# Kernel tuning notes

Hardware: AMD Instinct MI355X
Metric: run time of the kernel (lower is better)

Reference implementation:

```python
import jax, jax.numpy as jnp
import numpy as np
import math

Q_DIM = 1024
K_DIM = 1024
ATT_DIM = 1024
POS_DIM = 64
B, NQ, NK = 4, 2048, 2048
EPS = 1e-5


def _ln(x, g, b):
    m = jnp.mean(x, axis=-1, keepdims=True)
    v = jnp.var(x, axis=-1, keepdims=True)
    return (x - m) * jax.lax.rsqrt(v + EPS) * g + b


def _sinpos(n, dim):
    # SinPos: exp = 2*arange(dim//2)/dim; pos = p * 10000**-exp; cat(pos, pos+pi/2); sin
    e = 2.0 * jnp.arange(dim // 2, dtype=jnp.float32) / dim      # [dim/2]
    p = jnp.arange(n, dtype=jnp.float32)[:, None]                # [n,1]
    ph = p * jnp.power(10000.0, -e)[None, :]                     # [n,dim/2]
    return jnp.sin(jnp.concatenate([ph, ph + math.pi / 2], axis=1))  # [n,dim]


def setup_inputs() -> dict:
    key = jax.random.key(0)
    ks = jax.random.split(key, 8)
    s = 0.02
    return {
        "q": jax.random.normal(ks[0], (B, NQ, Q_DIM), jnp.float32),
        "k": jax.random.normal(ks[1], (B, NK, K_DIM), jnp.float32),
        "Wq": jax.random.normal(ks[2], (Q_DIM, ATT_DIM), jnp.float32) * s,
        "bq": jnp.zeros((ATT_DIM,), jnp.float32),
        "Wk": jax.random.normal(ks[3], (K_DIM, ATT_DIM), jnp.float32) * s,
        "bk": jnp.zeros((ATT_DIM,), jnp.float32),
        "Wv": jax.random.normal(ks[4], (K_DIM, ATT_DIM), jnp.float32) * s,
        "bv": jnp.zeros((ATT_DIM,), jnp.float32),
        "gq": jnp.ones((ATT_DIM,), jnp.float32), "betaq": jnp.zeros((ATT_DIM,), jnp.float32),
        "gk": jnp.ones((ATT_DIM,), jnp.float32), "betak": jnp.zeros((ATT_DIM,), jnp.float32),
        "gv": jnp.ones((ATT_DIM,), jnp.float32), "betav": jnp.zeros((ATT_DIM,), jnp.float32),
        "Wp": jax.random.normal(ks[5], (POS_DIM, POS_DIM), jnp.float32) * s,
        "bp": jnp.zeros((POS_DIM,), jnp.float32),
    }


def reference(q, k, Wq, bq, Wk, bk, Wv, bv, gq, betaq, gk, betak, gv, betav, Wp, bp):
    qn = _ln(q @ Wq + bq, gq, betaq)          # [B,NQ,D]
    vn = _ln(k @ Wv + bv, gv, betav)          # [B,NK,D]
    kn = _ln(k @ Wk + bk, gk, betak)          # [B,NK,D]
    pos = _sinpos(NK, POS_DIM)                # [NK,P]

    # attention 1: Q=qn, K=kn, V=pos
    s1 = jnp.einsum('bnd,bjd->bnj', qn, kn) * (1.0 / math.sqrt(ATT_DIM))
    a1 = jax.nn.softmax(s1, axis=-1)          # [B,NQ,NK]
    x = jnp.einsum('bnj,jp->bnp', a1, pos)    # [B,NQ,P]

    # pos_net (Linear)
    x = x @ Wp + bp                           # [B,NQ,P]

    # attention 2: Q=x, K=pos, V=vn
    s2 = jnp.einsum('bnp,jp->bnj', x, pos) * (1.0 / math.sqrt(POS_DIM))
    a2 = jax.nn.softmax(s2, axis=-1)          # [B,NQ,NK]
    out = jnp.einsum('bnj,bjd->bnd', a2, vn)  # [B,NQ,D]

    att = jnp.stack([a1, a2], axis=1)         # [B,2,NQ,NK] == torch.cat over head dim
    return out, att
```

## Files before the change

### kernel.cpp

```cpp
#include <hip/hip_runtime.h>
#include <math.h>
#include <stdint.h>


typedef _Float16 f16;
typedef _Float16 f16x4 __attribute__((ext_vector_type(4)));
typedef _Float16 f16x8 __attribute__((ext_vector_type(8)));
typedef float f32x4 __attribute__((ext_vector_type(4)));

static constexpr int CB  = 4;
static constexpr int CNQ = 2048;
static constexpr int CNK = 2048;
static constexpr int CD  = 1024;
static constexpr int CP  = 64;

static __device__ __forceinline__ void async16(const f16* gp, f16* lp) {
  __builtin_amdgcn_global_load_lds(
      (const __attribute__((address_space(1))) void*)(uintptr_t)gp,
      (__attribute__((address_space(3))) void*)(uint32_t)(uintptr_t)lp,
      16, 0, 0);
}

__global__ __launch_bounds__(256) void prep_kernel(
    const float* __restrict__ q, const float* __restrict__ k,
    const float* __restrict__ Wq, const float* __restrict__ Wk,
    const float* __restrict__ Wv,
    f16* __restrict__ q16, f16* __restrict__ k16,
    f16* __restrict__ WqT, f16* __restrict__ WkvT,
    f16* __restrict__ posb, f16* __restrict__ posTb) {
  const int b = blockIdx.x;
  if (b < 512) {
    int tid = b * 256 + threadIdx.x;
    int p = tid >> 11;
    int j = tid & (CNK - 1);
    int i = p & 31;
    float ph = (float)j * powf(10000.0f, -(float)i * (1.0f / 32.0f));
    float v = (p < 32) ? sinf(ph) : cosf(ph);
    posb[j * CP + p]   = (f16)v;
    posTb[p * CNK + j] = (f16)v;
  } else if (b < 512 + 16384) {
    const int NF4 = CB * CNQ * CD / 4;
    int tid = (b - 512) * 256 + threadIdx.x;
    const float* src = (tid < NF4) ? q : k;
    f16* dst = (tid < NF4) ? q16 : k16;
    int i = (tid < NF4) ? tid : tid - NF4;
    float4 v = reinterpret_cast<const float4*>(src)[i];
    f16x4 o = {(f16)v.x, (f16)v.y, (f16)v.z, (f16)v.w};
    reinterpret_cast<f16x4*>(dst)[i] = o;
  } else {
    __shared__ float t[64][65];
    const int idx = b - 16896;
    const int z = idx >> 8;
    const int rem = idx & 255;
    const float* W = (z == 0) ? Wq : (z == 1) ? Wk : Wv;
    f16* WT = (z == 0) ? WqT : (z == 1) ? WkvT : WkvT + 1024 * 1024;
    int k0 = (rem & 15) * 64, n0 = (rem >> 4) * 64;
    int tx = threadIdx.x & 63, ty = threadIdx.x >> 6;
#pragma unroll
    for (int i = 0; i < 16; i++)
      t[ty + 4 * i][tx] = W[(size_t)(k0 + ty + 4 * i) * CD + n0 + tx];
    __syncthreads();
#pragma unroll
    for (int i = 0; i < 16; i++)
      WT[(size_t)(n0 + 4 * i + ty) * CD + k0 + tx] = (f16)t[tx][ty + 4 * i];
  }
}

template <int BM, int BN>
__device__ __forceinline__ void gemm_core2(
    const f16* __restrict__ Ab, const f16* __restrict__ Bb,
    int lda, int ldb, int K, int m0, int n0, f16* sm,
    f32x4 (&acc)[BM / 32][4]) {
  constexpr int FM = BM / 32;
  constexpr int TI = (BM + BN) / 64;
  constexpr int bufsz = (BM + BN) * 64;
  const int tid = threadIdx.x;
  const int lane = tid & 63, wid = tid >> 6;
  const int wr = wid >> 2, wc = wid & 3;
  const int lrow = lane & 15, kg = lane >> 4;

  auto stage = [&](int i, int kt, int buf) {
    const int s = i * 512 + tid;
    const int row = s >> 3;
    const int cb = (s & 7) << 4;
    const int scb = cb ^ ((row & 7) << 4);
    const f16* src = (i < BM / 64)
        ? Ab + (size_t)(m0 + row) * lda + kt * 64 + (scb >> 1)
        : Bb + (size_t)(n0 + row - BM) * ldb + kt * 64 + (scb >> 1);
    async16(src, &sm[buf * bufsz + s * 8]);
  };

  const int NTk = K >> 6;
#pragma unroll
  for (int i = 0; i < TI; i++) stage(i, 0, 0);

  for (int t = 0; t < NTk; ++t) {
    const int cur = t & 1;
    if (t + 1 < NTk) {
#pragma unroll
      for (int i = 0; i < TI; i++) stage(i, t + 1, cur ^ 1);
      if constexpr (TI == 8) asm volatile("s_waitcnt vmcnt(8)" ::: "memory");
      else                   asm volatile("s_waitcnt vmcnt(6)" ::: "memory");
    } else {
      asm volatile("s_waitcnt vmcnt(0)" ::: "memory");
    }
    __builtin_amdgcn_s_barrier();

    const f16* smA = sm + cur * bufsz;
    const f16* smB = smA + BM * 64;
#pragma unroll
    for (int kk = 0; kk < 2; ++kk) {
      const int Cb = kk * 64 + kg * 16;
      f16x8 af[FM], bf[4];
#pragma unroll
      for (int m = 0; m < FM; ++m) {
        const int ar = wr * (BM / 2) + m * 16 + lrow;
        af[m] = *reinterpret_cast<const f16x8*>(
            &smA[ar * 64 + ((Cb ^ ((ar & 7) << 4)) >> 1)]);
      }
#pragma unroll
      for (int n = 0; n < 4; ++n) {
        const int br = wc * 64 + n * 16 + lrow;
        bf[n] = *reinterpret_cast<const f16x8*>(
            &smB[br * 64 + ((Cb ^ ((br & 7) << 4)) >> 1)]);
      }
      __builtin_amdgcn_s_barrier();
      __builtin_amdgcn_s_setprio(1);
#pragma unroll
      for (int m = 0; m < FM; ++m)
#pragma unroll
        for (int n = 0; n < 4; ++n)
          acc[m][n] = __builtin_amdgcn_mfma_f32_16x16x32_f16(af[m], bf[n], acc[m][n], 0, 0, 0);
      __builtin_amdgcn_s_setprio(0);
      __builtin_amdgcn_s_barrier();
    }
  }
}

template <int BM, int BN>
__device__ __forceinline__ void epi_f16(
    f32x4 (&acc)[BM / 32][4], f16* sm, f16* Cp, int ldc, int m0, int n0) {
  const int tid = threadIdx.x, lane = tid & 63, wid = tid >> 6;
  const int wr = wid >> 2, wc = wid & 3;
  const int rbase = wr * (BM / 2) + (lane >> 4) * 4;
  const int cbase = wc * 64 + (lane & 15);
  __syncthreads();
#pragma unroll
  for (int mg = 0; mg < BM / 32; mg++)
#pragma unroll
    for (int n = 0; n < 4; n++)
#pragma unroll
      for (int r = 0; r < 4; r++)
        sm[(rbase + mg * 16 + r) * BN + cbase + n * 16] = (f16)acc[mg][n][r];
  __syncthreads();
  constexpr int CH = BM * BN / (512 * 8);
#pragma unroll
  for (int c = 0; c < CH; c++) {
    const int idx = c * 512 + tid;
    const int row = idx / (BN / 8);
    const int cole = (idx % (BN / 8)) * 8;
    f16x8 v = *reinterpret_cast<const f16x8*>(&sm[row * BN + cole]);
    *reinterpret_cast<f16x8*>(Cp + (size_t)(m0 + row) * ldc + n0 + cole) = v;
  }
}

template <int BM, int BN>
__device__ __forceinline__ void epi_exp(
    f32x4 (&acc)[BM / 32][4], f16* sm, float* psum, f16* Cp, int ldc,
    int m0, int n0, float scale, float* PSrow) {
  constexpr int SL = BN / 8;
  const int tid = threadIdx.x, lane = tid & 63, wid = tid >> 6;
  const int wr = wid >> 2, wc = wid & 3;
  const int rbase = wr * (BM / 2) + (lane >> 4) * 4;
  const int cbase = wc * 64 + (lane & 15);
  __syncthreads();
#pragma unroll
  for (int mg = 0; mg < BM / 32; mg++)
#pragma unroll
    for (int n = 0; n < 4; n++)
#pragma unroll
      for (int r = 0; r < 4; r++)
        sm[(rbase + mg * 16 + r) * BN + cbase + n * 16] =
            (f16)__expf(acc[mg][n][r] * scale);
  __syncthreads();
  constexpr int CH = BM * BN / (512 * 8);
#pragma unroll
  for (int c = 0; c < CH; c++) {
    const int idx = c * 512 + tid;
    const int row = idx / SL;
    const int cole = (idx % SL) * 8;
    f16x8 v = *reinterpret_cast<const f16x8*>(&sm[row * BN + cole]);
    *reinterpret_cast<f16x8*>(Cp + (size_t)(m0 + row) * ldc + n0 + cole) = v;
    float p = 0.f;
#pragma unroll
    for (int j = 0; j < 8; j++) p += (float)v[j];
#pragma unroll
    for (int o = 1; o < SL; o <<= 1) p += __shfl_xor(p, o);
    if ((lane & (SL - 1)) == 0) psum[row] = p;
  }
  __syncthreads();
  if (tid < BM) PSrow[tid] = psum[tid];
}

template <int BM, int BN>
__device__ __forceinline__ void epi_f32(
    f32x4 (&acc)[BM / 32][4], f16* smh, float* Cp, int ldc, int m0, int n0) {
  float* st = (float*)smh;
  const int tid = threadIdx.x, lane = tid & 63, wid = tid >> 6;
  const int wr = wid >> 2, wc = wid & 3;
  const int cbase = wc * 64 + (lane & 15);
#pragma unroll
  for (int half = 0; half < 2; half++) {
    __syncthreads();
    if (wr == half) {
#pragma unroll
      for (int mg = 0; mg < BM / 32; mg++)
#pragma unroll
        for (int r = 0; r < 4; r++) {
          const int rloc = (lane >> 4) * 4 + mg * 16 + r;
#pragma unroll
          for (int n = 0; n < 4; n++)
            st[rloc * BN + cbase + n * 16] = acc[mg][n][r];
        }
    }
    __syncthreads();
    constexpr int CH = (BM / 2) * BN / (512 * 4);
#pragma unroll
    for (int c = 0; c < CH; c++) {
      const int idx = c * 512 + tid;
      const int row = idx / (BN / 4);
      const int cole = (idx % (BN / 4)) * 4;
      float4 v = *reinterpret_cast<const float4*>(&st[row * BN + cole]);
      *reinterpret_cast<float4*>(
          Cp + (size_t)(m0 + half * (BM / 2) + row) * ldc + n0 + cole) = v;
    }
  }
}

__global__ __launch_bounds__(512) void gemmIn_kernel(
    const f16* __restrict__ q16, const f16* __restrict__ WqT, f16* __restrict__ tmpq,
    const f16* __restrict__ k16, const f16* __restrict__ WkvT, f16* __restrict__ tmp2) {
  __shared__ __attribute__((aligned(16))) f16 sm[2 * (128 + 256) * 64];
  const int b = blockIdx.x;
  const int swz = (b & 7) * 96 + (b >> 3);
  const f16 *A, *B;
  f16* C;
  int ldc, m0, n0;
  if (swz < 256) {
    const int bx = swz & 63, by = swz >> 6;
    A = q16; B = WqT; C = tmpq; ldc = 1024; m0 = bx * 128; n0 = by * 256;
  } else {
    const int idx = swz - 256;
    const int bx = idx & 63, by = idx >> 6;
    A = k16; B = WkvT; C = tmp2; ldc = 2048; m0 = bx * 128; n0 = by * 256;
  }
  f32x4 acc[4][4] = {};
  gemm_core2<128, 256>(A, B, 1024, 1024, 1024, m0, n0, sm, acc);
  epi_f16<128, 256>(acc, sm, C, ldc, m0, n0);
}

__global__ __launch_bounds__(512) void gemmS1_kernel(
    const f16* __restrict__ qn, const f16* __restrict__ kn,
    f16* __restrict__ e1, float* __restrict__ PS) {
  __shared__ __attribute__((aligned(16))) f16 sm[2 * (256 + 256) * 64];
  __shared__ float psum[256];
  const int b = blockIdx.x;
  const int swz = (b & 7) * 32 + (b >> 3);
  const int bz = swz >> 6;
  const int rem = swz & 63;
  const int bx = rem & 7, by = rem >> 3;
  const int m0 = bx * 256, n0 = by * 256;
  const f16* Ab = qn + (size_t)bz * 2048 * 1024;
  const f16* Bb = kn + (size_t)bz * 2048 * 2048;
  f16* Cp = e1 + (size_t)bz * 2048 * 2048;
  f32x4 acc[8][4] = {};
  gemm_core2<256, 256>(Ab, Bb, 1024, 2048, 1024, m0, n0, sm, acc);
  epi_exp<256, 256>(acc, sm, psum, Cp, 2048, m0, n0, 0.03125f,
                    PS + (size_t)by * (CB * CNQ) + bz * 2048 + m0);
}

__global__ __launch_bounds__(512) void gemmOut_kernel(
    const f16* __restrict__ e2, const f16* __restrict__ vnT, float* __restrict__ out) {
  __shared__ __attribute__((aligned(16))) f16 sm[2 * (128 + 256) * 64];
  const int b = blockIdx.x;
  const int swz = (b & 7) * 32 + (b >> 3);
  const int bz = swz >> 6;
  const int rem = swz & 63;
  const int bx = rem & 15, by = rem >> 4;
  const int m0 = bx * 128, n0 = by * 256;
  const f16* Ab = e2 + (size_t)bz * 2048 * 2048;
  const f16* Bb = vnT + (size_t)bz * 1024 * 2048;
  float* Cp = out + (size_t)bz * 2048 * 1024;
  f32x4 acc[4][4] = {};
  gemm_core2<128, 256>(Ab, Bb, 2048, 2048, 2048, m0, n0, sm, acc);
  epi_f32<128, 256>(acc, sm, Cp, 1024, m0, n0);
}

__global__ __launch_bounds__(256) void ln3_kernel(
    f16* __restrict__ tmpq, f16* __restrict__ tmp2, float* __restrict__ vstat,
    const float* __restrict__ bq, const float* __restrict__ gq, const float* __restrict__ beq,
    const float* __restrict__ bk, const float* __restrict__ gk, const float* __restrict__ bek,
    const float* __restrict__ bv) {
  __shared__ float rs_[4], rq_[4];
  const int z = blockIdx.y;
  f16* rp;
  const float *bias, *g, *beta;
  if (z == 0)      { rp = tmpq + (size_t)blockIdx.x * 1024;        bias = bq; g = gq; beta = beq; }
  else if (z == 1) { rp = tmp2 + (size_t)blockIdx.x * 2048;        bias = bk; g = gk; beta = bek; }
  else             { rp = tmp2 + (size_t)blockIdx.x * 2048 + 1024; bias = bv; g = nullptr; beta = nullptr; }
  const int t = threadIdx.x;
  f16x4 v = *reinterpret_cast<const f16x4*>(rp + t * 4);
  float y[4], s = 0.f, q = 0.f;
#pragma unroll
  for (int j = 0; j < 4; j++) {
    y[j] = (float)v[j] + bias[t * 4 + j];
    s += y[j]; q += y[j] * y[j];
  }
#pragma unroll
  for (int o = 32; o; o >>= 1) { s += __shfl_xor(s, o); q += __shfl_xor(q, o); }
  if ((t & 63) == 0) { rs_[t >> 6] = s; rq_[t >> 6] = q; }
  __syncthreads();
  s = rs_[0] + rs_[1] + rs_[2] + rs_[3];
  q = rq_[0] + rq_[1] + rq_[2] + rq_[3];
  const float mean = s * (1.0f / CD);
  const float rstd = rsqrtf(q * (1.0f / CD) - mean * mean + 1e-5f);
  if (z == 2) {
    if (t == 0) { vstat[blockIdx.x] = mean; vstat[CB * CNK + blockIdx.x] = rstd; }
    return;
  }
  f16x4 o;
#pragma unroll
  for (int j = 0; j < 4; j++) {
    int c = t * 4 + j;
    o[j] = (f16)((y[j] - mean) * rstd * g[c] + beta[c]);
  }
  *reinterpret_cast<f16x4*>(rp + t * 4) = o;
}

__global__ __launch_bounds__(256) void transposeLN_kernel(
    const f16* __restrict__ tmp2, f16* __restrict__ vnT,
    const float* __restrict__ vstat, const float* __restrict__ bv,
    const float* __restrict__ gv, const float* __restrict__ bev) {
  __shared__ f16 t[64][65];
  __shared__ float ms[64], rs[64];
  int n0 = blockIdx.x * 64, d0 = blockIdx.y * 64;
  size_t ibase = (size_t)blockIdx.z * CNK * 2048;
  size_t obase = (size_t)blockIdx.z * CNK * CD;
  int tx = threadIdx.x & 63, ty = threadIdx.x >> 6;
  const int tokbase = blockIdx.z * CNK + n0;
  if (threadIdx.x < 64) {
    ms[threadIdx.x] = vstat[tokbase + threadIdx.x];
    rs[threadIdx.x] = vstat[CB * CNK + tokbase + threadIdx.x];
  }
#pragma unroll
  for (int i = 0; i < 16; i++)
    t[ty + 4 * i][tx] = tmp2[ibase + (size_t)(n0 + ty + 4 * i) * 2048 + 1024 + d0 + tx];
  __syncthreads();
#pragma unroll
  for (int i = 0; i < 16; i++) {
    const int dim = d0 + 4 * i + ty;
    const float yv = (float)t[tx][ty + 4 * i] + bv[dim];
    vnT[obase + (size_t)dim * CNK + n0 + tx] =
        (f16)((yv - ms[tx]) * rs[tx] * gv[dim] + bev[dim]);
  }
}

__global__ __launch_bounds__(256) void xgemm_kernel(
    const f16* __restrict__ e1, const f16* __restrict__ posTb,
    const float* __restrict__ PS, float* __restrict__ xw, float* __restrict__ att) {
  constexpr int BM = 64, BN = 64;
  __shared__ __attribute__((aligned(16))) f16 As[BM * 32];
  __shared__ __attribute__((aligned(16))) f16 Bs[BN * 32];
  __shared__ float invs[BM];
  const int tid = threadIdx.x;
  const int lane = tid & 63;
  const int wave = tid >> 6;
  const int wr = wave >> 1, wc = wave & 1;
  const int m0 = blockIdx.x * BM;
  const int kbase = blockIdx.z * 1024;
  const int srow = lane >> 2;
  const int scol = (lane & 3) * 8;
  const int lrow = lane & 15;
  const int kg = lane >> 4;

  if (tid < BM) {
    float s = 0.f;
#pragma unroll
    for (int j = 0; j < 8; j++) s += PS[j * (CB * CNQ) + m0 + tid];
    invs[tid] = 1.0f / s;
  }

  const int bb = m0 >> 11, nloc = m0 & (CNQ - 1);
  float* attb = att + ((size_t)(bb << 1) * CNQ + nloc) * CNK + kbase;
  const int arow = tid >> 2, acol = (tid & 3) * 8;

  f32x4 acc[2][2] = {};
  for (int k0 = 0; k0 < 1024; k0 += 32) {
    __syncthreads();
#pragma unroll
    for (int i = wave; i < 8; i += 4) {
      if (i < 4)
        async16(e1 + (size_t)(m0 + i * 16 + srow) * CNK + kbase + k0 + scol, &As[i * 512]);
      else
        async16(posTb + (size_t)((i - 4) * 16 + srow) * CNK + kbase + k0 + scol,
                &Bs[(i - 4) * 512]);
    }
    __syncthreads();
    f16x8 af[2], bfr[2];
#pragma unroll
    for (int m = 0; m < 2; m++)
      af[m] = *reinterpret_cast<const f16x8*>(&As[(wr * 32 + m * 16 + lrow) * 32 + kg * 8]);
#pragma unroll
    for (int n = 0; n < 2; n++)
      bfr[n] = *reinterpret_cast<const f16x8*>(&Bs[(wc * 32 + n * 16 + lrow) * 32 + kg * 8]);
#pragma unroll
    for (int m = 0; m < 2; m++)
#pragma unroll
      for (int n = 0; n < 2; n++)
        acc[m][n] = __builtin_amdgcn_mfma_f32_16x16x32_f16(af[m], bfr[n], acc[m][n], 0, 0, 0);
    {
      const float iv = invs[arow];
      f16x8 v = *reinterpret_cast<const f16x8*>(&As[arow * 32 + acol]);
      float4 w0 = {(float)v[0] * iv, (float)v[1] * iv, (float)v[2] * iv, (float)v[3] * iv};
      float4 w1 = {(float)v[4] * iv, (float)v[5] * iv, (float)v[6] * iv, (float)v[7] * iv};
      float* ap = attb + (size_t)arow * CNK + k0 + acol;
      reinterpret_cast<float4*>(ap)[0] = w0;
      reinterpret_cast<float4*>(ap)[1] = w1;
    }
  }
  float* Cp = xw + (size_t)blockIdx.z * (CB * CNQ) * CP;
  const int crow = m0 + wr * 32 + (lane >> 4) * 4;
  const int ccol = wc * 32 + (lane & 15);
#pragma unroll
  for (int m = 0; m < 2; m++)
#pragma unroll
    for (int n = 0; n < 2; n++)
#pragma unroll
      for (int r = 0; r < 4; r++)
        Cp[(size_t)(crow + m * 16 + r) * CP + ccol + n * 16] = acc[m][n][r];
}

__global__ __launch_bounds__(512) void attn2_kernel(
    const float* __restrict__ xw, const float* __restrict__ Wp,
    const float* __restrict__ bp, const f16* __restrict__ posb,
    const float* __restrict__ PS, f16* __restrict__ e2,
    float* __restrict__ att) {
  __shared__ __attribute__((aligned(16))) f16 shm[32 * 2048 + 32 * 64];
  __shared__ float rsum4[4][32];
  __shared__ float invs[32];
  f16* e2lds = shm;
  f16* xpb = shm + 32 * 2048;
  float* xs = (float*)shm;
  float* Wps = (float*)shm + 32 * 64;
  const int tid = threadIdx.x, l = tid & 63, w = tid >> 6;
  const int r0 = blockIdx.x * 32;
  if (tid < 32) {
    float s = 0.f;
#pragma unroll
    for (int j = 0; j < 8; j++) s += PS[j * (CB * CNQ) + r0 + tid];
    invs[tid] = 1.0f / s;
  }
  __syncthreads();
  if (w < 2) {
#pragma unroll
    for (int i = 0; i < 16; i++) {
      const int row = w * 16 + i;
      const size_t gi = (size_t)(r0 + row) * CP + l;
      xs[row * 64 + l] = (xw[gi] + xw[(size_t)(CB * CNQ) * CP + gi]) * invs[row];
    }
#pragma unroll
    for (int i = w; i < 64; i += 2) Wps[i * 64 + l] = Wp[i * 64 + l];
  }
  const float bpl = bp[l];
  __syncthreads();
  if (w < 2) {
#pragma unroll 2
    for (int i = 0; i < 16; i++) {
      float a = bpl;
#pragma unroll 8
      for (int p = 0; p < 64; p++) a = fmaf(xs[(w * 16 + i) * 64 + p], Wps[p * 64 + l], a);
      xpb[(w * 16 + i) * 64 + l] = (f16)a;
    }
  }
  __syncthreads();
  const int rb = (w & 1) * 16, jh = w >> 1;
  const f16x8 af0 = *reinterpret_cast<const f16x8*>(&xpb[(rb + (l & 15)) * 64 + (l >> 4) * 8]);
  const f16x8 af1 = *reinterpret_cast<const f16x8*>(&xpb[(rb + (l & 15)) * 64 + 32 + (l >> 4) * 8]);
  float rs[4] = {0.f, 0.f, 0.f, 0.f};
  for (int jt = jh * 8; jt < jh * 8 + 8; jt++) {
#pragma unroll
    for (int q4 = 0; q4 < 4; q4++) {
      const int j = jt * 64 + q4 * 16 + (l & 15);
      const f16* pp = posb + (size_t)j * CP + (l >> 4) * 8;
      f16x8 b0 = *reinterpret_cast<const f16x8*>(pp);
      f16x8 b1 = *reinterpret_cast<const f16x8*>(pp + 32);
      f32x4 c = {};
      c = __builtin_amdgcn_mfma_f32_16x16x32_f16(af0, b0, c, 0, 0, 0);
      c = __builtin_amdgcn_mfma_f32_16x16x32_f16(af1, b1, c, 0, 0, 0);
#pragma unroll
      for (int r = 0; r < 4; r++) {
        float ev = __expf(c[r] * 0.125f);
        rs[r] += ev;
        e2lds[(rb + (l >> 4) * 4 + r) * 2048 + j] = (f16)ev;
      }
    }
  }
#pragma unroll
  for (int r = 0; r < 4; r++) {
#pragma unroll
    for (int o = 1; o < 16; o <<= 1) rs[r] += __shfl_xor(rs[r], o);
    if ((l & 15) == 0) rsum4[jh][rb + (l >> 4) * 4 + r] = rs[r];
  }
  __syncthreads();
  const int b = r0 >> 11, nloc = r0 & (CNQ - 1);
  float* attb = att + ((size_t)((b << 1) + 1) * CNQ + nloc) * CNK;
  f16* e2b = e2 + (size_t)r0 * CNK;
  for (int it = 0; it < 8; it++) {
    const int row = it * 4 + (tid >> 7);
    const int col = (tid & 127) * 16;
    const float iv = 1.0f / (rsum4[0][row] + rsum4[1][row] + rsum4[2][row] + rsum4[3][row]);
    const f16x8 a0 = *reinterpret_cast<const f16x8*>(&e2lds[row * 2048 + col]);
    const f16x8 a1 = *reinterpret_cast<const f16x8*>(&e2lds[row * 2048 + col + 8]);
    float4 w0 = {(float)a0[0] * iv, (float)a0[1] * iv, (float)a0[2] * iv, (float)a0[3] * iv};
    float4 w1 = {(float)a0[4] * iv, (float)a0[5] * iv, (float)a0[6] * iv, (float)a0[7] * iv};
    float4 w2 = {(float)a1[0] * iv, (float)a1[1] * iv, (float)a1[2] * iv, (float)a1[3] * iv};
    float4 w3 = {(float)a1[4] * iv, (float)a1[5] * iv, (float)a1[6] * iv, (float)a1[7] * iv};
    float* ap = attb + (size_t)row * CNK + col;
    reinterpret_cast<float4*>(ap)[0] = w0;
    reinterpret_cast<float4*>(ap)[1] = w1;
    reinterpret_cast<float4*>(ap)[2] = w2;
    reinterpret_cast<float4*>(ap)[3] = w3;
    f16x8 h0 = {(f16)w0.x, (f16)w0.y, (f16)w0.z, (f16)w0.w,
                (f16)w1.x, (f16)w1.y, (f16)w1.z, (f16)w1.w};
    f16x8 h1 = {(f16)w2.x, (f16)w2.y, (f16)w2.z, (f16)w2.w,
                (f16)w3.x, (f16)w3.y, (f16)w3.z, (f16)w3.w};
    f16* ep = e2b + (size_t)row * CNK + col;
    *reinterpret_cast<f16x8*>(ep)     = h0;
    *reinterpret_cast<f16x8*>(ep + 8) = h1;
  }
}

extern "C" void kernel_launch(void* const* d_in, const int* in_sizes, int n_in,
                              void* d_out, int out_size, void* d_ws, size_t ws_size,
                              hipStream_t stream) {
  (void)in_sizes; (void)n_in; (void)out_size; (void)ws_size;
  const float* q    = (const float*)d_in[0];
  const float* k    = (const float*)d_in[1];
  const float* Wq   = (const float*)d_in[2];
  const float* bq   = (const float*)d_in[3];
  const float* Wk   = (const float*)d_in[4];
  const float* bk   = (const float*)d_in[5];
  const float* Wv   = (const float*)d_in[6];
  const float* bv   = (const float*)d_in[7];
  const float* gq   = (const float*)d_in[8];
  const float* betaq= (const float*)d_in[9];
  const float* gk   = (const float*)d_in[10];
  const float* betak= (const float*)d_in[11];
  const float* gv   = (const float*)d_in[12];
  const float* betav= (const float*)d_in[13];
  const float* Wp   = (const float*)d_in[14];
  const float* bp   = (const float*)d_in[15];

  float* out = (float*)d_out;
  float* att = out + (size_t)CB * CNQ * CD;
  char* ws = (char*)d_ws;
  const size_t MB = 1ull << 20;

  f16* q16   = (f16*)(ws);
  f16* k16   = (f16*)(ws + 16 * MB);
  f16* e1    = (f16*)(ws);
  f16* e2    = (f16*)(ws);
  f16* WqT   = (f16*)(ws + 32 * MB);
  f16* WkvT  = (f16*)(ws + 34 * MB);
  f16* posb  = (f16*)(ws + 38 * MB);
  f16* posTb = (f16*)(ws + 38 * MB + 256 * 1024);
  float* xw  = (float*)(ws + 38 * MB + 512 * 1024);
  float* PS  = (float*)(ws + 42 * MB + 512 * 1024);
  float* vstat = (float*)(ws + 42 * MB + 768 * 1024);
  f16* tmpq  = (f16*)(ws + 43 * MB);
  f16* tmp2  = (f16*)(ws + 59 * MB);
  f16* vnT   = (f16*)(ws + 91 * MB);
  f16* qn = tmpq;
  f16* kn = tmp2;

  prep_kernel<<<512 + 16384 + 768, 256, 0, stream>>>(
      q, k, Wq, Wk, Wv, q16, k16, WqT, WkvT, posb, posTb);

  gemmIn_kernel<<<768, 512, 0, stream>>>(q16, WqT, tmpq, k16, WkvT, tmp2);
  ln3_kernel<<<dim3(CB * CNQ, 3), 256, 0, stream>>>(
      tmpq, tmp2, vstat, bq, gq, betaq, bk, gk, betak, bv);
  transposeLN_kernel<<<dim3(CNK / 64, CD / 64, CB), 256, 0, stream>>>(
      tmp2, vnT, vstat, bv, gv, betav);

  gemmS1_kernel<<<256, 512, 0, stream>>>(qn, kn, e1, PS);

  xgemm_kernel<<<dim3(CB * CNQ / 64, 1, 2), 256, 0, stream>>>(e1, posTb, PS, xw, att);
  attn2_kernel<<<CB * CNQ / 32, 512, 0, stream>>>(xw, Wp, bp, posb, PS, e2, att);

  gemmOut_kernel<<<256, 512, 0, stream>>>(e2, vnT, out);
}
```

Before: 292.5 us.

## Double-buffer xgemm, use nontemporal att stores, trim GEMM mainloop barriers

Rewrites xgemm to 512 threads with a swizzled, double-buffered async LDS pipeline over 64-wide K tiles. The normalized att1 write now happens after the GEMM and re-reads e1 from global memory instead of LDS. The shared GEMM mainloop drops the per-kk barriers and sets priority once per K tile. The fp32 attention and GEMM epilogue writes become nontemporal stores to reduce cache pollution, at the cost of a second read of e1 in xgemm.

New measurement: 326.4 us. +11.6%, slower.

```diff
diff --git a/kernel.cpp b/kernel.cpp
--- a/kernel.cpp
+++ b/kernel.cpp
@@ -108,6 +108,7 @@
 
     const f16* smA = sm + cur * bufsz;
     const f16* smB = smA + BM * 64;
+    __builtin_amdgcn_s_setprio(1);
 #pragma unroll
     for (int kk = 0; kk < 2; ++kk) {
       const int Cb = kk * 64 + kg * 16;
@@ -124,16 +125,14 @@
         bf[n] = *reinterpret_cast<const f16x8*>(
             &smB[br * 64 + ((Cb ^ ((br & 7) << 4)) >> 1)]);
       }
-      __builtin_amdgcn_s_barrier();
-      __builtin_amdgcn_s_setprio(1);
 #pragma unroll
       for (int m = 0; m < FM; ++m)
 #pragma unroll
         for (int n = 0; n < 4; ++n)
           acc[m][n] = __builtin_amdgcn_mfma_f32_16x16x32_f16(af[m], bf[n], acc[m][n], 0, 0, 0);
-      __builtin_amdgcn_s_setprio(0);
-      __builtin_amdgcn_s_barrier();
-    }
+    }
+    __builtin_amdgcn_s_setprio(0);
+    __builtin_amdgcn_s_barrier();
   }
 }
 
@@ -230,9 +229,9 @@
       const int idx = c * 512 + tid;
       const int row = idx / (BN / 4);
       const int cole = (idx % (BN / 4)) * 4;
-      float4 v = *reinterpret_cast<const float4*>(&st[row * BN + cole]);
-      *reinterpret_cast<float4*>(
-          Cp + (size_t)(m0 + half * (BM / 2) + row) * ldc + n0 + cole) = v;
+      f32x4 v = *reinterpret_cast<const f32x4*>(&st[row * BN + cole]);
+      __builtin_nontemporal_store(v, reinterpret_cast<f32x4*>(
+          Cp + (size_t)(m0 + half * (BM / 2) + row) * ldc + n0 + cole));
     }
   }
 }
@@ -365,79 +364,94 @@
   }
 }
 
-__global__ __launch_bounds__(256) void xgemm_kernel(
+__global__ __launch_bounds__(512) void xgemm_kernel(
     const f16* __restrict__ e1, const f16* __restrict__ posTb,
     const float* __restrict__ PS, float* __restrict__ xw, float* __restrict__ att) {
-  constexpr int BM = 64, BN = 64;
-  __shared__ __attribute__((aligned(16))) f16 As[BM * 32];
-  __shared__ __attribute__((aligned(16))) f16 Bs[BN * 32];
-  __shared__ float invs[BM];
-  const int tid = threadIdx.x;
-  const int lane = tid & 63;
-  const int wave = tid >> 6;
-  const int wr = wave >> 1, wc = wave & 1;
-  const int m0 = blockIdx.x * BM;
+  __shared__ __attribute__((aligned(16))) f16 sm[2 * 128 * 64];
+  __shared__ float invs[64];
+  const int tid = threadIdx.x, lane = tid & 63, wid = tid >> 6;
+  const int wr = wid >> 1, wc = wid & 1;
+  const int lrow = lane & 15, kg = lane >> 4;
+  const int m0 = blockIdx.x * 64;
   const int kbase = blockIdx.z * 1024;
-  const int srow = lane >> 2;
-  const int scol = (lane & 3) * 8;
-  const int lrow = lane & 15;
-  const int kg = lane >> 4;
-
-  if (tid < BM) {
+
+  if (tid < 64) {
     float s = 0.f;
 #pragma unroll
     for (int j = 0; j < 8; j++) s += PS[j * (CB * CNQ) + m0 + tid];
     invs[tid] = 1.0f / s;
   }
 
+  auto stage = [&](int i, int kt, int buf) {
+    const int s = i * 512 + tid;
+    const int row = s >> 3;
+    const int cb = (s & 7) << 4;
+    const int scb = cb ^ ((row & 7) << 4);
+    const f16* src = (row < 64)
+        ? e1 + (size_t)(m0 + row) * CNK + kbase + kt * 64 + (scb >> 1)
+        : posTb + (size_t)(row - 64) * CNK + kbase + kt * 64 + (scb >> 1);
+    async16(src, &sm[buf * (128 * 64) + s * 8]);
+  };
+
+  f32x4 acc[2] = {};
+  const int NTk = 16;
+#pragma unroll
+  for (int i = 0; i < 2; i++) stage(i, 0, 0);
+
+  for (int t = 0; t < NTk; ++t) {
+    const int cur = t & 1;
+    if (t + 1 < NTk) {
+#pragma unroll
+      for (int i = 0; i < 2; i++) stage(i, t + 1, cur ^ 1);
+      asm volatile("s_waitcnt vmcnt(2)" ::: "memory");
+    } else {
+      asm volatile("s_waitcnt vmcnt(0)" ::: "memory");
+    }
+    __builtin_amdgcn_s_barrier();
+    const f16* smA = sm + cur * (128 * 64);
+    const f16* smB = smA + 64 * 64;
+#pragma unroll
+    for (int kk = 0; kk < 2; ++kk) {
+      const int Cb = kk * 64 + kg * 16;
+      const int ar = wr * 16 + lrow;
+      f16x8 af = *reinterpret_cast<const f16x8*>(
+          &smA[ar * 64 + ((Cb ^ ((ar & 7) << 4)) >> 1)]);
+#pragma unroll
+      for (int n = 0; n < 2; ++n) {
+        const int br = wc * 32 + n * 16 + lrow;
+        f16x8 bf = *reinterpret_cast<const f16x8*>(
+            &smB[br * 64 + ((Cb ^ ((br & 7) << 4)) >> 1)]);
+        acc[n] = __builtin_amdgcn_mfma_f32_16x16x32_f16(af, bf, acc[n], 0, 0, 0);
+      }
+    }
+    __builtin_amdgcn_s_barrier();
+  }
+
+  float* Cp = xw + (size_t)blockIdx.z * (CB * CNQ) * CP;
+  const int crow = m0 + wr * 16 + (lane >> 4) * 4;
+  const int ccol = wc * 32 + (lane & 15);
+#pragma unroll
+  for (int n = 0; n < 2; n++)
+#pragma unroll
+    for (int r = 0; r < 4; r++)
+      Cp[(size_t)(crow + r) * CP + ccol + n * 16] = acc[n][r];
+
   const int bb = m0 >> 11, nloc = m0 & (CNQ - 1);
   float* attb = att + ((size_t)(bb << 1) * CNQ + nloc) * CNK + kbase;
-  const int arow = tid >> 2, acol = (tid & 3) * 8;
-
-  f32x4 acc[2][2] = {};
-  for (int k0 = 0; k0 < 1024; k0 += 32) {
-    __syncthreads();
-#pragma unroll
-    for (int i = wave; i < 8; i += 4) {
-      if (i < 4)
-        async16(e1 + (size_t)(m0 + i * 16 + srow) * CNK + kbase + k0 + scol, &As[i * 512]);
-      else
-        async16(posTb + (size_t)((i - 4) * 16 + srow) * CNK + kbase + k0 + scol,
-                &Bs[(i - 4) * 512]);
-    }
-    __syncthreads();
-    f16x8 af[2], bfr[2];
-#pragma unroll
-    for (int m = 0; m < 2; m++)
-      af[m] = *reinterpret_cast<const f16x8*>(&As[(wr * 32 + m * 16 + lrow) * 32 + kg * 8]);
-#pragma unroll
-    for (int n = 0; n < 2; n++)
-      bfr[n] = *reinterpret_cast<const f16x8*>(&Bs[(wc * 32 + n * 16 + lrow) * 32 + kg * 8]);
-#pragma unroll
-    for (int m = 0; m < 2; m++)
-#pragma unroll
-      for (int n = 0; n < 2; n++)
-        acc[m][n] = __builtin_amdgcn_mfma_f32_16x16x32_f16(af[m], bfr[n], acc[m][n], 0, 0, 0);
-    {
-      const float iv = invs[arow];
-      f16x8 v = *reinterpret_cast<const f16x8*>(&As[arow * 32 + acol]);
-      float4 w0 = {(float)v[0] * iv, (float)v[1] * iv, (float)v[2] * iv, (float)v[3] * iv};
-      float4 w1 = {(float)v[4] * iv, (float)v[5] * iv, (float)v[6] * iv, (float)v[7] * iv};
-      float* ap = attb + (size_t)arow * CNK + k0 + acol;
-      reinterpret_cast<float4*>(ap)[0] = w0;
-      reinterpret_cast<float4*>(ap)[1] = w1;
-    }
-  }
-  float* Cp = xw + (size_t)blockIdx.z * (CB * CNQ) * CP;
-  const int crow = m0 + wr * 32 + (lane >> 4) * 4;
-  const int ccol = wc * 32 + (lane & 15);
-#pragma unroll
-  for (int m = 0; m < 2; m++)
-#pragma unroll
-    for (int n = 0; n < 2; n++)
-#pragma unroll
-      for (int r = 0; r < 4; r++)
-        Cp[(size_t)(crow + m * 16 + r) * CP + ccol + n * 16] = acc[m][n][r];
+#pragma unroll
+  for (int c = 0; c < 16; c++) {
+    const int idx = c * 512 + tid;
+    const int row = idx >> 7;
+    const int col = (idx & 127) * 8;
+    const float iv = invs[row];
+    f16x8 v = *reinterpret_cast<const f16x8*>(
+        &e1[(size_t)(m0 + row) * CNK + kbase + col]);
+    f32x4 w0 = {(float)v[0] * iv, (float)v[1] * iv, (float)v[2] * iv, (float)v[3] * iv};
+    f32x4 w1 = {(float)v[4] * iv, (float)v[5] * iv, (float)v[6] * iv, (float)v[7] * iv};
+    float* ap = attb + (size_t)row * CNK + col;
+    __builtin_nontemporal_store(w0, reinterpret_cast<f32x4*>(ap));
+    __builtin_nontemporal_store(w1, reinterpret_cast<f32x4*>(ap) + 1);
+  }
 }
 
 __global__ __launch_bounds__(512) void attn2_kernel(
@@ -521,19 +535,19 @@
     const float iv = 1.0f / (rsum4[0][row] + rsum4[1][row] + rsum4[2][row] + rsum4[3][row]);
     const f16x8 a0 = *reinterpret_cast<const f16x8*>(&e2lds[row * 2048 + col]);
     const f16x8 a1 = *reinterpret_cast<const f16x8*>(&e2lds[row * 2048 + col + 8]);
-    float4 w0 = {(float)a0[0] * iv, (float)a0[1] * iv, (float)a0[2] * iv, (float)a0[3] * iv};
-    float4 w1 = {(float)a0[4] * iv, (float)a0[5] * iv, (float)a0[6] * iv, (float)a0[7] * iv};
-    float4 w2 = {(float)a1[0] * iv, (float)a1[1] * iv, (float)a1[2] * iv, (float)a1[3] * iv};
-    float4 w3 = {(float)a1[4] * iv, (float)a1[5] * iv, (float)a1[6] * iv, (float)a1[7] * iv};
+    f32x4 w0 = {(float)a0[0] * iv, (float)a0[1] * iv, (float)a0[2] * iv, (float)a0[3] * iv};
+    f32x4 w1 = {(float)a0[4] * iv, (float)a0[5] * iv, (float)a0[6] * iv, (float)a0[7] * iv};
+    f32x4 w2 = {(float)a1[0] * iv, (float)a1[1] * iv, (float)a1[2] * iv, (float)a1[3] * iv};
+    f32x4 w3 = {(float)a1[4] * iv, (float)a1[5] * iv, (float)a1[6] * iv, (float)a1[7] * iv};
     float* ap = attb + (size_t)row * CNK + col;
-    reinterpret_cast<float4*>(ap)[0] = w0;
-    reinterpret_cast<float4*>(ap)[1] = w1;
-    reinterpret_cast<float4*>(ap)[2] = w2;
-    reinterpret_cast<float4*>(ap)[3] = w3;
-    f16x8 h0 = {(f16)w0.x, (f16)w0.y, (f16)w0.z, (f16)w0.w,
-                (f16)w1.x, (f16)w1.y, (f16)w1.z, (f16)w1.w};
-    f16x8 h1 = {(f16)w2.x, (f16)w2.y, (f16)w2.z, (f16)w2.w,
-                (f16)w3.x, (f16)w3.y, (f16)w3.z, (f16)w3.w};
+    __builtin_nontemporal_store(w0, reinterpret_cast<f32x4*>(ap));
+    __builtin_nontemporal_store(w1, reinterpret_cast<f32x4*>(ap) + 1);
+    __builtin_nontemporal_store(w2, reinterpret_cast<f32x4*>(ap) + 2);
+    __builtin_nontemporal_store(w3, reinterpret_cast<f32x4*>(ap) + 3);
+    f16x8 h0 = {(f16)w0[0], (f16)w0[1], (f16)w0[2], (f16)w0[3],
+                (f16)w1[0], (f16)w1[1], (f16)w1[2], (f16)w1[3]};
+    f16x8 h1 = {(f16)w2[0], (f16)w2[1], (f16)w2[2], (f16)w2[3],
+                (f16)w3[0], (f16)w3[1], (f16)w3[2], (f16)w3[3]};
     f16* ep = e2b + (size_t)row * CNK + col;
     *reinterpret_cast<f16x8*>(ep)     = h0;
     *reinterpret_cast<f16x8*>(ep + 8) = h1;
@@ -594,7 +608,7 @@
 
   gemmS1_kernel<<<256, 512, 0, stream>>>(qn, kn, e1, PS);
 
-  xgemm_kernel<<<dim3(CB * CNQ / 64, 1, 2), 256, 0, stream>>>(e1, posTb, PS, xw, att);
+  xgemm_kernel<<<dim3(CB * CNQ / 64, 1, 2), 512, 0, stream>>>(e1, posTb, PS, xw, att);
   attn2_kernel<<<CB * CNQ / 32, 512, 0, stream>>>(xw, Wp, bp, posb, PS, e2, att);
 
   gemmOut_kernel<<<256, 512, 0, stream>>>(e2, vnT, out);
```
